# Kernel optimization log

Measured on AMD Instinct MI355X. Metric: run time of the kernel, lower is better.

The kernel has to match this reference:

```python
import jax, jax.numpy as jnp
import numpy as np

NUM_EDGE_TYPES = 8
HIDDEN = 128
N_NODES = 50000
N_EDGES = 600000


def setup_inputs() -> dict:
    key = jax.random.key(0)
    ks = jax.random.split(key, 10)
    H = HIDDEN
    h = jax.random.normal(ks[0], (N_NODES, H), dtype=jnp.float32)
    edge_index = jax.random.randint(ks[1], (2, N_EDGES), 0, N_NODES, dtype=jnp.int32)
    edge_type = jax.random.randint(ks[2], (N_EDGES,), 0, NUM_EDGE_TYPES + 1, dtype=jnp.int32)
    s = 1.0 / np.sqrt(H)
    W_msg = jax.random.uniform(ks[3], (H, H), jnp.float32, -s, s)
    b_msg = jax.random.uniform(ks[4], (H,), jnp.float32, -s, s)
    edge_embed = jax.random.normal(ks[5], (NUM_EDGE_TYPES + 1, H), dtype=jnp.float32)
    W_ih = jax.random.uniform(ks[6], (3 * H, H), jnp.float32, -s, s)
    W_hh = jax.random.uniform(ks[7], (3 * H, H), jnp.float32, -s, s)
    b_ih = jax.random.uniform(ks[8], (3 * H,), jnp.float32, -s, s)
    b_hh = jax.random.uniform(ks[9], (3 * H,), jnp.float32, -s, s)
    return {"h": h, "edge_index": edge_index, "edge_type": edge_type,
            "num_nodes": N_NODES, "W_msg": W_msg, "b_msg": b_msg,
            "edge_embed": edge_embed, "W_ih": W_ih, "W_hh": W_hh,
            "b_ih": b_ih, "b_hh": b_hh}


def _gru_cell(x, h, W_ih, W_hh, b_ih, b_hh):
    # PyTorch GRUCell: gates ordered (r, z, n)
    H = h.shape[-1]
    gi = x @ W_ih.T + b_ih  # (N, 3H)
    gh = h @ W_hh.T + b_hh
    i_r, i_z, i_n = gi[:, :H], gi[:, H:2 * H], gi[:, 2 * H:]
    h_r, h_z, h_n = gh[:, :H], gh[:, H:2 * H], gh[:, 2 * H:]
    r = jax.nn.sigmoid(i_r + h_r)
    z = jax.nn.sigmoid(i_z + h_z)
    n = jnp.tanh(i_n + r * h_n)
    return (1.0 - z) * n + z * h


def reference(h, edge_index, edge_type, num_nodes, W_msg, b_msg, edge_embed, W_ih, W_hh, b_ih, b_hh):
    src = edge_index[0]
    dst = edge_index[1]
    # gather -> linear -> edge-type embed add
    src_h = h[src] @ W_msg.T + b_msg                      # (E, H)
    emb = edge_embed[jnp.clip(edge_type, 0, NUM_EDGE_TYPES)]  # (E, H)
    msg = src_h + emb
    # scatter-add into per-node message buffer
    messages = jax.ops.segment_sum(msg, dst, num_segments=num_nodes)  # (num_nodes, H)
    h_new = _gru_cell(messages, h[:num_nodes], W_ih, W_hh, b_ih, b_hh)
    result = jnp.zeros_like(h).at[:num_nodes].set(h_new)
    return result
```

## Files before the change

kernel.cpp:

```cpp
#include <hip/hip_runtime.h>
#include <math.h>

#define H 128
typedef unsigned int u32;
typedef unsigned long long u64;
typedef __attribute__((ext_vector_type(8))) short short8;
typedef __attribute__((ext_vector_type(4))) float floatx4;

#define XS_STRIDE 136
#define CS_STRIDE 40

#define SCAN_B 64
#define SCAN_T 256

__device__ __forceinline__ float sigmoid_f(float x) {
    return 1.0f / (1.0f + __expf(-x));
}
__device__ __forceinline__ float tanh_f(float x) {
    float t = __expf(-2.0f * fabsf(x));
    float r = (1.0f - t) / (1.0f + t);
    return copysignf(r, x);
}
__device__ __forceinline__ unsigned short f2bf(float x) {
    u32 u = __float_as_uint(x);
    return (unsigned short)((u + 0x7fffu + ((u >> 16) & 1u)) >> 16);
}
__device__ __forceinline__ float bf2f(unsigned short s) {
    return __uint_as_float(((u32)s) << 16);
}
__device__ __forceinline__ float bf_lo32(u32 u) { return __uint_as_float(u << 16); }
__device__ __forceinline__ float bf_hi32(u32 u) { return __uint_as_float(u & 0xffff0000u); }

__global__ __launch_bounds__(256) void fused_pre_kernel(
    const float* __restrict__ h, unsigned short* __restrict__ h_b, int total8,
    int* __restrict__ deg, int N,
    const float* __restrict__ Wih, const float* __restrict__ Whh,
    const float* __restrict__ Wm,  const float* __restrict__ emb,
    const float* __restrict__ bm,
    unsigned short* __restrict__ Wcs, unsigned short* __restrict__ Whhs,
    unsigned short* __restrict__ embWs, int HB, int DB)
{
    int b = blockIdx.x;
    if (b < HB) {
        int idx = b * 256 + threadIdx.x;
        if (idx >= total8) return;
        const float4* p = (const float4*)(h + (size_t)idx * 8);
        float4 a = p[0], bb = p[1];
        short8 v;
        v[0] = (short)f2bf(a.x);  v[1] = (short)f2bf(a.y);
        v[2] = (short)f2bf(a.z);  v[3] = (short)f2bf(a.w);
        v[4] = (short)f2bf(bb.x); v[5] = (short)f2bf(bb.y);
        v[6] = (short)f2bf(bb.z); v[7] = (short)f2bf(bb.w);
        *(short8*)(h_b + (size_t)idx * 8) = v;
        return;
    }
    if (b < HB + DB) {
        int idx = (b - HB) * 256 + threadIdx.x;
        if (idx < N) deg[idx] = 0;
        return;
    }
    int idx = (b - HB - DB) * 256 + threadIdx.x;
    if (idx < 49152) {
        int g = idx >> 7;
        int k = idx & 127;
        float acc = 0.f;
#pragma unroll 4
        for (int c = 0; c < H; ++c)
            acc += Wih[(size_t)g * H + c] * Wm[(size_t)c * H + k];
        int gate = g >> 7;
        int wi = g & 127;
        int j = wi >> 4, m = wi & 15;
        int kc = k >> 5, q = (k >> 3) & 3, i = k & 7;
        int l = q * 16 + m;
        Wcs[(size_t)(((gate * 8 + j) * 4 + kc) * 64 + l) * 8 + i] = f2bf(acc);
    } else if (idx < 61440) {
        int s = idx - 49152;
        int i = s & 7;
        int l = (s >> 3) & 63;
        int jb = s >> 9;
        int gate = jb >> 3, jj = jb & 7;
        int q = l >> 4, m = l & 15;
        int t = q * 8 + i;
        unsigned short v = 0;
        if (t < 9) {
            int g = gate * 128 + jj * 16 + m;
            float acc = 0.f;
#pragma unroll 4
            for (int jx = 0; jx < H; ++jx)
                acc += (emb[(size_t)t * H + jx] + bm[jx]) * Wih[(size_t)g * H + jx];
            v = f2bf(acc);
        }
        embWs[s] = v;
    } else if (idx < 67584) {
        int t2 = idx - 61440;
        int l  = t2 & 63;
        int kc = (t2 >> 6) & 3;
        int jr = t2 >> 8;
        int m = l & 15, q = l >> 4;
        size_t srco = (size_t)(jr * 16 + m) * H + kc * 32 + q * 8;
        const float4* s0 = (const float4*)(Whh + srco);
        float4 a = s0[0], bb = s0[1];
        short8 v;
        v[0] = (short)f2bf(a.x);  v[1] = (short)f2bf(a.y);
        v[2] = (short)f2bf(a.z);  v[3] = (short)f2bf(a.w);
        v[4] = (short)f2bf(bb.x); v[5] = (short)f2bf(bb.y);
        v[6] = (short)f2bf(bb.z); v[7] = (short)f2bf(bb.w);
        *(short8*)(Whhs + (size_t)t2 * 8) = v;
    }
}

__global__ __launch_bounds__(256) void hist_kernel(
    const int* __restrict__ eidx, int* __restrict__ deg, int E)
{
    int e = blockIdx.x * 256 + threadIdx.x;
    if (e < E) atomicAdd(&deg[eidx[E + e]], 1);
}

__global__ __launch_bounds__(SCAN_T) void scan_part_kernel(
    const int* __restrict__ deg, int* __restrict__ tsum,
    int* __restrict__ bsum, int N, int ipt)
{
    __shared__ int red[SCAN_T];
    int t = threadIdx.x;
    int g = blockIdx.x * SCAN_T + t;
    int s = g * ipt;
    int e = s + ipt < N ? s + ipt : N;
    int sum = 0;
    for (int i = s; i < e; ++i) sum += deg[i];
    tsum[g] = sum;
    red[t] = sum;
    __syncthreads();
    for (int d = SCAN_T / 2; d > 0; d >>= 1) {
        if (t < d) red[t] += red[t + d];
        __syncthreads();
    }
    if (t == 0) bsum[blockIdx.x] = red[0];
}

__global__ __launch_bounds__(SCAN_T) void scan_final_kernel(
    const int* __restrict__ deg, const int* __restrict__ tsum,
    const int* __restrict__ bsum, int* __restrict__ off,
    int* __restrict__ pos, int N, int ipt)
{
    __shared__ int part[SCAN_T];
    __shared__ int bpre[SCAN_B + 1];
    int t = threadIdx.x;
    if (t == 0) {
        int acc = 0;
        for (int b2 = 0; b2 < SCAN_B; ++b2) { bpre[b2] = acc; acc += bsum[b2]; }
        bpre[SCAN_B] = acc;
        if (blockIdx.x == 0) off[N] = acc;
    }
    int g = blockIdx.x * SCAN_T + t;
    part[t] = tsum[g];
    __syncthreads();
    for (int d = 1; d < SCAN_T; d <<= 1) {
        int v = (t >= d) ? part[t - d] : 0;
        __syncthreads();
        part[t] += v;
        __syncthreads();
    }
    int base = bpre[blockIdx.x] + ((t == 0) ? 0 : part[t - 1]);
    int s = g * ipt;
    int e = s + ipt < N ? s + ipt : N;
    for (int i = s; i < e; ++i) {
        off[i] = base;
        pos[i] = base;
        base += deg[i];
    }
}

__global__ __launch_bounds__(256) void fill_kernel(
    const int* __restrict__ eidx, const int* __restrict__ etype,
    int* __restrict__ pos, int* __restrict__ packed, int E)
{
    int e = blockIdx.x * 256 + threadIdx.x;
    if (e >= E) return;
    int src = eidx[e];
    int dst = eidx[E + e];
    int t = etype[e];
    t = t < 0 ? 0 : (t > 8 ? 8 : t);
    int p = atomicAdd(&pos[dst], 1);
    packed[p] = src | (t << 24);
}

__global__ __launch_bounds__(256) void gather_kernel(
    const unsigned short* __restrict__ h_b,
    const int* __restrict__ off, const int* __restrict__ packed,
    unsigned short* __restrict__ S_b, u64* __restrict__ cnt, int N)
{
    int n = blockIdx.x * 4 + (threadIdx.x >> 6);
    if (n >= N) return;
    int lane = threadIdx.x & 63;
    int b = off[n], e = off[n + 1];
    float ax = 0.f, ay = 0.f;
    u64 c = 0;
    int i = b;
    for (; i + 8 <= e; i += 8) {
        int u0 = packed[i + 0];
        int u1 = packed[i + 1];
        int u2 = packed[i + 2];
        int u3 = packed[i + 3];
        int u4 = packed[i + 4];
        int u5 = packed[i + 5];
        int u6 = packed[i + 6];
        int u7 = packed[i + 7];
        u32 x0 = *((const u32*)(h_b + (size_t)(u0 & 0xffffff) * H) + lane);
        u32 x1 = *((const u32*)(h_b + (size_t)(u1 & 0xffffff) * H) + lane);
        u32 x2 = *((const u32*)(h_b + (size_t)(u2 & 0xffffff) * H) + lane);
        u32 x3 = *((const u32*)(h_b + (size_t)(u3 & 0xffffff) * H) + lane);
        u32 x4 = *((const u32*)(h_b + (size_t)(u4 & 0xffffff) * H) + lane);
        u32 x5 = *((const u32*)(h_b + (size_t)(u5 & 0xffffff) * H) + lane);
        u32 x6 = *((const u32*)(h_b + (size_t)(u6 & 0xffffff) * H) + lane);
        u32 x7 = *((const u32*)(h_b + (size_t)(u7 & 0xffffff) * H) + lane);
        c += (1ull << (7 * (u0 >> 24))) + (1ull << (7 * (u1 >> 24)))
           + (1ull << (7 * (u2 >> 24))) + (1ull << (7 * (u3 >> 24)))
           + (1ull << (7 * (u4 >> 24))) + (1ull << (7 * (u5 >> 24)))
           + (1ull << (7 * (u6 >> 24))) + (1ull << (7 * (u7 >> 24)));
        ax += bf_lo32(x0) + bf_lo32(x1) + bf_lo32(x2) + bf_lo32(x3)
            + bf_lo32(x4) + bf_lo32(x5) + bf_lo32(x6) + bf_lo32(x7);
        ay += bf_hi32(x0) + bf_hi32(x1) + bf_hi32(x2) + bf_hi32(x3)
            + bf_hi32(x4) + bf_hi32(x5) + bf_hi32(x6) + bf_hi32(x7);
    }
    for (; i + 4 <= e; i += 4) {
        int u0 = packed[i + 0];
        int u1 = packed[i + 1];
        int u2 = packed[i + 2];
        int u3 = packed[i + 3];
        u32 x0 = *((const u32*)(h_b + (size_t)(u0 & 0xffffff) * H) + lane);
        u32 x1 = *((const u32*)(h_b + (size_t)(u1 & 0xffffff) * H) + lane);
        u32 x2 = *((const u32*)(h_b + (size_t)(u2 & 0xffffff) * H) + lane);
        u32 x3 = *((const u32*)(h_b + (size_t)(u3 & 0xffffff) * H) + lane);
        c += (1ull << (7 * (u0 >> 24))) + (1ull << (7 * (u1 >> 24)))
           + (1ull << (7 * (u2 >> 24))) + (1ull << (7 * (u3 >> 24)));
        ax += bf_lo32(x0) + bf_lo32(x1) + bf_lo32(x2) + bf_lo32(x3);
        ay += bf_hi32(x0) + bf_hi32(x1) + bf_hi32(x2) + bf_hi32(x3);
    }
    for (; i < e; ++i) {
        int u = packed[i];
        u32 x = *((const u32*)(h_b + (size_t)(u & 0xffffff) * H) + lane);
        c += 1ull << (7 * (u >> 24));
        ax += bf_lo32(x);
        ay += bf_hi32(x);
    }
    u32 o = (u32)f2bf(ax) | ((u32)f2bf(ay) << 16);
    *((u32*)(S_b + (size_t)n * H) + lane) = o;
    if (lane == 0) cnt[n] = c;
}

__global__ __launch_bounds__(256, 4) void gru_mfma_kernel(
    const unsigned short* __restrict__ S_b, const unsigned short* __restrict__ h_b,
    const unsigned short* __restrict__ Wcs, const unsigned short* __restrict__ Whhs,
    const unsigned short* __restrict__ embWs,
    const float* __restrict__ bih, const float* __restrict__ bhh,
    const u64* __restrict__ cnt,
    const int* __restrict__ numn, float* __restrict__ out, int N)
{
    __shared__ unsigned short xs[64 * XS_STRIDE];
    __shared__ unsigned short hsb[64 * XS_STRIDE];
    __shared__ unsigned short cs[64 * CS_STRIDE];

    int tid = threadIdx.x;
    int bx = blockIdx.x;
    int node0 = (bx >> 1) * 64;
    int jhalf = bx & 1;

    int lane = tid & 63;
    int wv = tid >> 6;
    int j = jhalf * 4 + wv;

    short8 er = *(const short8*)(embWs + (size_t)((0 * 8 + j) * 64 + lane) * 8);
    short8 ez = *(const short8*)(embWs + (size_t)((1 * 8 + j) * 64 + lane) * 8);
    short8 en = *(const short8*)(embWs + (size_t)((2 * 8 + j) * 64 + lane) * 8);

    for (int c = tid; c < 1024; c += 256) {
        int r = c >> 4;
        int k8 = (c & 15) << 3;
        int n = node0 + r;
        int nc = n < N ? n : N - 1;
        *(short8*)(&xs[r * XS_STRIDE + k8]) =
            *(const short8*)(S_b + (size_t)nc * H + k8);
        *(short8*)(&hsb[r * XS_STRIDE + k8]) =
            *(const short8*)(h_b + (size_t)nc * H + k8);
    }
    {
        int r = tid >> 2, tg = tid & 3;
        int n = node0 + r;
        u64 cv = cnt[n < N ? n : N - 1];
        short8 v = {0, 0, 0, 0, 0, 0, 0, 0};
        if (tg == 0) {
#pragma unroll
            for (int i = 0; i < 8; ++i)
                v[i] = (short)f2bf((float)((u32)(cv >> (7 * i)) & 127u));
        } else if (tg == 1) {
            v[0] = (short)f2bf((float)((u32)(cv >> 56) & 127u));
        }
        *(short8*)(&cs[r * CS_STRIDE + tg * 8]) = v;
    }
    __syncthreads();

    int am = lane & 15;
    int aq = lane >> 4;

    int num_nodes = numn[0];
    floatx4 zero = {0.f, 0.f, 0.f, 0.f};

    floatx4 aR[4], aZ[4], aIn[4], aHn[4];
#pragma unroll
    for (int rt = 0; rt < 4; ++rt) {
        short8 acn = *(const short8*)(&cs[(rt * 16 + am) * CS_STRIDE + aq * 8]);
        aR[rt]  = __builtin_amdgcn_mfma_f32_16x16x32_bf16(acn, er, zero, 0, 0, 0);
        aZ[rt]  = __builtin_amdgcn_mfma_f32_16x16x32_bf16(acn, ez, zero, 0, 0, 0);
        aIn[rt] = __builtin_amdgcn_mfma_f32_16x16x32_bf16(acn, en, zero, 0, 0, 0);
        aHn[rt] = zero;
    }
#pragma unroll
    for (int kc = 0; kc < 4; ++kc) {
        size_t c_r = (size_t)(((0 * 8 + j) * 4 + kc) * 64 + lane) * 8;
        size_t c_z = (size_t)(((1 * 8 + j) * 4 + kc) * 64 + lane) * 8;
        size_t c_n = (size_t)(((2 * 8 + j) * 4 + kc) * 64 + lane) * 8;
        short8 bir = *(const short8*)(Wcs + c_r);
        short8 bhr = *(const short8*)(Whhs + c_r);
        short8 biz = *(const short8*)(Wcs + c_z);
        short8 bhz = *(const short8*)(Whhs + c_z);
        short8 bin = *(const short8*)(Wcs + c_n);
        short8 bhn = *(const short8*)(Whhs + c_n);
#pragma unroll
        for (int rt = 0; rt < 4; ++rt) {
            int arow = rt * 16 + am;
            short8 axv = *(const short8*)(&xs[arow * XS_STRIDE + kc * 32 + aq * 8]);
            short8 ahv = *(const short8*)(&hsb[arow * XS_STRIDE + kc * 32 + aq * 8]);
            aR[rt]  = __builtin_amdgcn_mfma_f32_16x16x32_bf16(axv, bir, aR[rt], 0, 0, 0);
            aR[rt]  = __builtin_amdgcn_mfma_f32_16x16x32_bf16(ahv, bhr, aR[rt], 0, 0, 0);
            aZ[rt]  = __builtin_amdgcn_mfma_f32_16x16x32_bf16(axv, biz, aZ[rt], 0, 0, 0);
            aZ[rt]  = __builtin_amdgcn_mfma_f32_16x16x32_bf16(ahv, bhz, aZ[rt], 0, 0, 0);
            aIn[rt] = __builtin_amdgcn_mfma_f32_16x16x32_bf16(axv, bin, aIn[rt], 0, 0, 0);
            aHn[rt] = __builtin_amdgcn_mfma_f32_16x16x32_bf16(ahv, bhn, aHn[rt], 0, 0, 0);
        }
    }
    int c = j * 16 + am;
    float b_r = bih[c]       + bhh[c];
    float b_z = bih[128 + c] + bhh[128 + c];
    float b_in = bih[256 + c], b_hn = bhh[256 + c];
#pragma unroll
    for (int rt = 0; rt < 4; ++rt) {
#pragma unroll
        for (int q = 0; q < 4; ++q) {
            int m = rt * 16 + aq * 4 + q;
            int node = node0 + m;
            if (node < N) {
                float r  = sigmoid_f(aR[rt][q] + b_r);
                float z  = sigmoid_f(aZ[rt][q] + b_z);
                float nv = tanh_f((aIn[rt][q] + b_in) + r * (aHn[rt][q] + b_hn));
                float hv = bf2f(hsb[m * XS_STRIDE + c]);
                float o  = (1.0f - z) * nv + z * hv;
                out[(size_t)node * H + c] = (node < num_nodes) ? o : 0.0f;
            }
        }
    }
}

extern "C" void kernel_launch(void* const* d_in, const int* in_sizes, int n_in,
                              void* d_out, int out_size, void* d_ws, size_t ws_size,
                              hipStream_t stream) {
    const float* h    = (const float*)d_in[0];
    const int*  eidx  = (const int*)d_in[1];
    const int*  etype = (const int*)d_in[2];
    const int*  numn  = (const int*)d_in[3];
    const float* Wm   = (const float*)d_in[4];
    const float* bm   = (const float*)d_in[5];
    const float* emb  = (const float*)d_in[6];
    const float* Wih  = (const float*)d_in[7];
    const float* Whh  = (const float*)d_in[8];
    const float* bih  = (const float*)d_in[9];
    const float* bhh  = (const float*)d_in[10];

    int N = in_sizes[0] / H;
    int E = in_sizes[2];

    unsigned short* S_b   = (unsigned short*)d_ws;
    unsigned short* h_b   = S_b + (size_t)N * H;
    unsigned short* Wcs   = h_b + (size_t)N * H;
    unsigned short* Whhs  = Wcs + 3 * H * H;
    unsigned short* embWs = Whhs + 3 * H * H;
    u64* cnt    = (u64*)(embWs + 12288);
    int* deg    = (int*)(cnt + N);
    int* pos    = deg + N;
    int* off    = pos + N;
    int* packed = off + (N + 1);
    int* tsum   = packed + E;
    int* bsum   = tsum + SCAN_B * SCAN_T;

    int total8 = N * H / 8;
    int HB = (total8 + 255) / 256;
    int DB = (N + 255) / 256;
    int PB = 264;
    fused_pre_kernel<<<HB + DB + PB, 256, 0, stream>>>(
        h, h_b, total8, deg, N, Wih, Whh, Wm, emb, bm, Wcs, Whhs, embWs, HB, DB);

    hist_kernel<<<(E + 255) / 256, 256, 0, stream>>>(eidx, deg, E);

    int ipt = (N + SCAN_B * SCAN_T - 1) / (SCAN_B * SCAN_T);
    scan_part_kernel<<<SCAN_B, SCAN_T, 0, stream>>>(deg, tsum, bsum, N, ipt);
    scan_final_kernel<<<SCAN_B, SCAN_T, 0, stream>>>(deg, tsum, bsum, off, pos, N, ipt);

    fill_kernel<<<(E + 255) / 256, 256, 0, stream>>>(eidx, etype, pos, packed, E);

    gather_kernel<<<(N + 3) / 4, 256, 0, stream>>>(h_b, off, packed, S_b, cnt, N);

    int nblk = ((N + 63) / 64) * 2;
    gru_mfma_kernel<<<nblk, 256, 0, stream>>>(S_b, h_b, Wcs, Whhs, embWs,
                                              bih, bhh, cnt, numn, (float*)d_out, N);
}
```

Measured before the change: 225.9 us.

## Fuse all stages into one cooperative persistent kernel with grid syncs

Replaces the seven separate launches (bf16 convert, histogram, two scan kernels, CSR fill, gather, GRU) with a single cooperative mega-kernel. It runs a grid-stride loop per stage, separated by grid.sync, and restructures the scan to use per-block sums. This removes per-launch overhead and inter-kernel gaps. The cost is a persistent grid of at most 512 blocks with launch bounds of 2 blocks per CU, which may lower occupancy for the memory-bound gather and GRU stages, plus several grid-wide barriers. The old multi-kernel path is kept as a fallback if the cooperative launch fails.

```diff
diff --git a/kernel.cpp b/kernel.cpp
--- a/kernel.cpp
+++ b/kernel.cpp
@@ -1,5 +1,8 @@
 #include <hip/hip_runtime.h>
+#include <hip/hip_cooperative_groups.h>
 #include <math.h>
+
+namespace cg = cooperative_groups;
 
 #define H 128
 typedef unsigned int u32;
@@ -31,35 +34,28 @@
 __device__ __forceinline__ float bf_lo32(u32 u) { return __uint_as_float(u << 16); }
 __device__ __forceinline__ float bf_hi32(u32 u) { return __uint_as_float(u & 0xffff0000u); }
 
-__global__ __launch_bounds__(256) void fused_pre_kernel(
-    const float* __restrict__ h, unsigned short* __restrict__ h_b, int total8,
-    int* __restrict__ deg, int N,
+
+__device__ __forceinline__ void conv8_item(
+    int idx, const float* __restrict__ h, unsigned short* __restrict__ h_b)
+{
+    const float4* p = (const float4*)(h + (size_t)idx * 8);
+    float4 a = p[0], bb = p[1];
+    short8 v;
+    v[0] = (short)f2bf(a.x);  v[1] = (short)f2bf(a.y);
+    v[2] = (short)f2bf(a.z);  v[3] = (short)f2bf(a.w);
+    v[4] = (short)f2bf(bb.x); v[5] = (short)f2bf(bb.y);
+    v[6] = (short)f2bf(bb.z); v[7] = (short)f2bf(bb.w);
+    *(short8*)(h_b + (size_t)idx * 8) = v;
+}
+
+__device__ __forceinline__ void prep_item(
+    int idx,
     const float* __restrict__ Wih, const float* __restrict__ Whh,
     const float* __restrict__ Wm,  const float* __restrict__ emb,
     const float* __restrict__ bm,
     unsigned short* __restrict__ Wcs, unsigned short* __restrict__ Whhs,
-    unsigned short* __restrict__ embWs, int HB, int DB)
-{
-    int b = blockIdx.x;
-    if (b < HB) {
-        int idx = b * 256 + threadIdx.x;
-        if (idx >= total8) return;
-        const float4* p = (const float4*)(h + (size_t)idx * 8);
-        float4 a = p[0], bb = p[1];
-        short8 v;
-        v[0] = (short)f2bf(a.x);  v[1] = (short)f2bf(a.y);
-        v[2] = (short)f2bf(a.z);  v[3] = (short)f2bf(a.w);
-        v[4] = (short)f2bf(bb.x); v[5] = (short)f2bf(bb.y);
-        v[6] = (short)f2bf(bb.z); v[7] = (short)f2bf(bb.w);
-        *(short8*)(h_b + (size_t)idx * 8) = v;
-        return;
-    }
-    if (b < HB + DB) {
-        int idx = (b - HB) * 256 + threadIdx.x;
-        if (idx < N) deg[idx] = 0;
-        return;
-    }
-    int idx = (b - HB - DB) * 256 + threadIdx.x;
+    unsigned short* __restrict__ embWs)
+{
     if (idx < 49152) {
         int g = idx >> 7;
         int k = idx & 127;
@@ -109,89 +105,12 @@
     }
 }
 
-__global__ __launch_bounds__(256) void hist_kernel(
-    const int* __restrict__ eidx, int* __restrict__ deg, int E)
-{
-    int e = blockIdx.x * 256 + threadIdx.x;
-    if (e < E) atomicAdd(&deg[eidx[E + e]], 1);
-}
-
-__global__ __launch_bounds__(SCAN_T) void scan_part_kernel(
-    const int* __restrict__ deg, int* __restrict__ tsum,
-    int* __restrict__ bsum, int N, int ipt)
-{
-    __shared__ int red[SCAN_T];
-    int t = threadIdx.x;
-    int g = blockIdx.x * SCAN_T + t;
-    int s = g * ipt;
-    int e = s + ipt < N ? s + ipt : N;
-    int sum = 0;
-    for (int i = s; i < e; ++i) sum += deg[i];
-    tsum[g] = sum;
-    red[t] = sum;
-    __syncthreads();
-    for (int d = SCAN_T / 2; d > 0; d >>= 1) {
-        if (t < d) red[t] += red[t + d];
-        __syncthreads();
-    }
-    if (t == 0) bsum[blockIdx.x] = red[0];
-}
-
-__global__ __launch_bounds__(SCAN_T) void scan_final_kernel(
-    const int* __restrict__ deg, const int* __restrict__ tsum,
-    const int* __restrict__ bsum, int* __restrict__ off,
-    int* __restrict__ pos, int N, int ipt)
-{
-    __shared__ int part[SCAN_T];
-    __shared__ int bpre[SCAN_B + 1];
-    int t = threadIdx.x;
-    if (t == 0) {
-        int acc = 0;
-        for (int b2 = 0; b2 < SCAN_B; ++b2) { bpre[b2] = acc; acc += bsum[b2]; }
-        bpre[SCAN_B] = acc;
-        if (blockIdx.x == 0) off[N] = acc;
-    }
-    int g = blockIdx.x * SCAN_T + t;
-    part[t] = tsum[g];
-    __syncthreads();
-    for (int d = 1; d < SCAN_T; d <<= 1) {
-        int v = (t >= d) ? part[t - d] : 0;
-        __syncthreads();
-        part[t] += v;
-        __syncthreads();
-    }
-    int base = bpre[blockIdx.x] + ((t == 0) ? 0 : part[t - 1]);
-    int s = g * ipt;
-    int e = s + ipt < N ? s + ipt : N;
-    for (int i = s; i < e; ++i) {
-        off[i] = base;
-        pos[i] = base;
-        base += deg[i];
-    }
-}
-
-__global__ __launch_bounds__(256) void fill_kernel(
-    const int* __restrict__ eidx, const int* __restrict__ etype,
-    int* __restrict__ pos, int* __restrict__ packed, int E)
-{
-    int e = blockIdx.x * 256 + threadIdx.x;
-    if (e >= E) return;
-    int src = eidx[e];
-    int dst = eidx[E + e];
-    int t = etype[e];
-    t = t < 0 ? 0 : (t > 8 ? 8 : t);
-    int p = atomicAdd(&pos[dst], 1);
-    packed[p] = src | (t << 24);
-}
-
-__global__ __launch_bounds__(256) void gather_kernel(
+__device__ __forceinline__ void gather_node(
+    int n, int lane,
     const unsigned short* __restrict__ h_b,
     const int* __restrict__ off, const int* __restrict__ packed,
-    unsigned short* __restrict__ S_b, u64* __restrict__ cnt, int N)
-{
-    int n = blockIdx.x * 4 + (threadIdx.x >> 6);
-    if (n >= N) return;
-    int lane = threadIdx.x & 63;
+    unsigned short* __restrict__ S_b, u64* __restrict__ cnt)
+{
     int b = off[n], e = off[n + 1];
     float ax = 0.f, ay = 0.f;
     u64 c = 0;
@@ -248,26 +167,21 @@
     if (lane == 0) cnt[n] = c;
 }
 
-__global__ __launch_bounds__(256, 4) void gru_mfma_kernel(
+__device__ __forceinline__ void gru_unit(
+    int node0, int jhalf, int tid,
+    unsigned short* xs, unsigned short* hsb, unsigned short* cs,
     const unsigned short* __restrict__ S_b, const unsigned short* __restrict__ h_b,
     const unsigned short* __restrict__ Wcs, const unsigned short* __restrict__ Whhs,
     const unsigned short* __restrict__ embWs,
     const float* __restrict__ bih, const float* __restrict__ bhh,
-    const u64* __restrict__ cnt,
-    const int* __restrict__ numn, float* __restrict__ out, int N)
-{
-    __shared__ unsigned short xs[64 * XS_STRIDE];
-    __shared__ unsigned short hsb[64 * XS_STRIDE];
-    __shared__ unsigned short cs[64 * CS_STRIDE];
-
-    int tid = threadIdx.x;
-    int bx = blockIdx.x;
-    int node0 = (bx >> 1) * 64;
-    int jhalf = bx & 1;
-
+    const u64* __restrict__ cnt, int num_nodes,
+    float* __restrict__ out, int N)
+{
     int lane = tid & 63;
     int wv = tid >> 6;
     int j = jhalf * 4 + wv;
+
+    __syncthreads();
 
     short8 er = *(const short8*)(embWs + (size_t)((0 * 8 + j) * 64 + lane) * 8);
     short8 ez = *(const short8*)(embWs + (size_t)((1 * 8 + j) * 64 + lane) * 8);
@@ -302,9 +216,7 @@
     int am = lane & 15;
     int aq = lane >> 4;
 
-    int num_nodes = numn[0];
     floatx4 zero = {0.f, 0.f, 0.f, 0.f};
-
     floatx4 aR[4], aZ[4], aIn[4], aHn[4];
 #pragma unroll
     for (int rt = 0; rt < 4; ++rt) {
@@ -360,6 +272,248 @@
     }
 }
 
+__global__ __launch_bounds__(256, 2) void mega_kernel(
+    const float* __restrict__ h, unsigned short* __restrict__ h_b, int total8,
+    const int* __restrict__ eidx, const int* __restrict__ etype, int E,
+    int* __restrict__ deg, int* __restrict__ off, int* __restrict__ pos,
+    int* __restrict__ packed, int* __restrict__ mbsum, int* __restrict__ mbpre,
+    const float* __restrict__ Wih, const float* __restrict__ Whh,
+    const float* __restrict__ Wm,  const float* __restrict__ emb,
+    const float* __restrict__ bm,
+    unsigned short* __restrict__ Wcs, unsigned short* __restrict__ Whhs,
+    unsigned short* __restrict__ embWs,
+    unsigned short* __restrict__ S_b, u64* __restrict__ cnt,
+    const float* __restrict__ bih, const float* __restrict__ bhh,
+    const int* __restrict__ numn, float* __restrict__ out, int N)
+{
+    __shared__ unsigned short xs[64 * XS_STRIDE];
+    __shared__ unsigned short hsb[64 * XS_STRIDE];
+    __shared__ unsigned short cs[64 * CS_STRIDE];
+
+    cg::grid_group grid = cg::this_grid();
+    int tid = threadIdx.x;
+    int nb  = gridDim.x;
+    int T   = nb * 256;
+    int gid = blockIdx.x * 256 + tid;
+
+    for (int idx = gid; idx < total8; idx += T) conv8_item(idx, h, h_b);
+    for (int idx = gid; idx < N; idx += T) deg[idx] = 0;
+    for (int idx = gid; idx < 67584; idx += T)
+        prep_item(idx, Wih, Whh, Wm, emb, bm, Wcs, Whhs, embWs);
+    __threadfence();
+    grid.sync();
+
+    for (int e = gid; e < E; e += T) atomicAdd(&deg[eidx[E + e]], 1);
+    __threadfence();
+    grid.sync();
+
+    int ipt = (N + T - 1) / T;
+    int* sscan = (int*)xs;
+    {
+        int s = gid * ipt;
+        int en = s + ipt < N ? s + ipt : N;
+        int sum = 0;
+        for (int i = s; i < en; ++i) sum += deg[i];
+        sscan[tid] = sum;
+        __syncthreads();
+        for (int d = 1; d < 256; d <<= 1) {
+            int v = (tid >= d) ? sscan[tid - d] : 0;
+            __syncthreads();
+            sscan[tid] += v;
+            __syncthreads();
+        }
+        if (tid == 255) mbsum[blockIdx.x] = sscan[255];
+    }
+    __threadfence();
+    grid.sync();
+
+    if (blockIdx.x == 0) {
+        int* ps = (int*)hsb;
+        int b0 = (2 * tid     < nb) ? mbsum[2 * tid]     : 0;
+        int b1 = (2 * tid + 1 < nb) ? mbsum[2 * tid + 1] : 0;
+        ps[tid] = b0 + b1;
+        __syncthreads();
+        for (int d = 1; d < 256; d <<= 1) {
+            int v = (tid >= d) ? ps[tid - d] : 0;
+            __syncthreads();
+            ps[tid] += v;
+            __syncthreads();
+        }
+        int excl_pair = tid ? ps[tid - 1] : 0;
+        if (2 * tid     < nb) mbpre[2 * tid]     = excl_pair;
+        if (2 * tid + 1 < nb) mbpre[2 * tid + 1] = excl_pair + b0;
+        if (tid == 255) off[N] = ps[255];
+    }
+    __threadfence();
+    grid.sync();
+
+    {
+        int base = mbpre[blockIdx.x] + (tid ? sscan[tid - 1] : 0);
+        int s = gid * ipt;
+        int en = s + ipt < N ? s + ipt : N;
+        for (int i = s; i < en; ++i) {
+            off[i] = base;
+            pos[i] = base;
+            base += deg[i];
+        }
+    }
+    __threadfence();
+    grid.sync();
+
+    for (int e = gid; e < E; e += T) {
+        int src = eidx[e];
+        int dst = eidx[E + e];
+        int t = etype[e];
+        t = t < 0 ? 0 : (t > 8 ? 8 : t);
+        int p = atomicAdd(&pos[dst], 1);
+        packed[p] = src | (t << 24);
+    }
+    __threadfence();
+    grid.sync();
+
+    {
+        int lane = tid & 63, wv = tid >> 6;
+        for (int n = blockIdx.x * 4 + wv; n < N; n += nb * 4)
+            gather_node(n, lane, h_b, off, packed, S_b, cnt);
+    }
+    __threadfence();
+    grid.sync();
+
+    {
+        int num_nodes = numn[0];
+        int nunits = ((N + 63) / 64) * 2;
+        for (int u = blockIdx.x; u < nunits; u += nb)
+            gru_unit((u >> 1) * 64, u & 1, tid, xs, hsb, cs,
+                     S_b, h_b, Wcs, Whhs, embWs, bih, bhh, cnt,
+                     num_nodes, out, N);
+    }
+}
+
+__global__ __launch_bounds__(256) void fused_pre_kernel(
+    const float* __restrict__ h, unsigned short* __restrict__ h_b, int total8,
+    int* __restrict__ deg, int N,
+    const float* __restrict__ Wih, const float* __restrict__ Whh,
+    const float* __restrict__ Wm,  const float* __restrict__ emb,
+    const float* __restrict__ bm,
+    unsigned short* __restrict__ Wcs, unsigned short* __restrict__ Whhs,
+    unsigned short* __restrict__ embWs, int HB, int DB)
+{
+    int b = blockIdx.x;
+    if (b < HB) {
+        int idx = b * 256 + threadIdx.x;
+        if (idx < total8) conv8_item(idx, h, h_b);
+        return;
+    }
+    if (b < HB + DB) {
+        int idx = (b - HB) * 256 + threadIdx.x;
+        if (idx < N) deg[idx] = 0;
+        return;
+    }
+    int idx = (b - HB - DB) * 256 + threadIdx.x;
+    prep_item(idx, Wih, Whh, Wm, emb, bm, Wcs, Whhs, embWs);
+}
+
+__global__ __launch_bounds__(256) void hist_kernel(
+    const int* __restrict__ eidx, int* __restrict__ deg, int E)
+{
+    int e = blockIdx.x * 256 + threadIdx.x;
+    if (e < E) atomicAdd(&deg[eidx[E + e]], 1);
+}
+
+__global__ __launch_bounds__(SCAN_T) void scan_part_kernel(
+    const int* __restrict__ deg, int* __restrict__ tsum,
+    int* __restrict__ bsum, int N, int ipt)
+{
+    __shared__ int red[SCAN_T];
+    int t = threadIdx.x;
+    int g = blockIdx.x * SCAN_T + t;
+    int s = g * ipt;
+    int e = s + ipt < N ? s + ipt : N;
+    int sum = 0;
+    for (int i = s; i < e; ++i) sum += deg[i];
+    tsum[g] = sum;
+    red[t] = sum;
+    __syncthreads();
+    for (int d = SCAN_T / 2; d > 0; d >>= 1) {
+        if (t < d) red[t] += red[t + d];
+        __syncthreads();
+    }
+    if (t == 0) bsum[blockIdx.x] = red[0];
+}
+
+__global__ __launch_bounds__(SCAN_T) void scan_final_kernel(
+    const int* __restrict__ deg, const int* __restrict__ tsum,
+    const int* __restrict__ bsum, int* __restrict__ off,
+    int* __restrict__ pos, int N, int ipt)
+{
+    __shared__ int part[SCAN_T];
+    __shared__ int bpre[SCAN_B + 1];
+    int t = threadIdx.x;
+    if (t == 0) {
+        int acc = 0;
+        for (int b2 = 0; b2 < SCAN_B; ++b2) { bpre[b2] = acc; acc += bsum[b2]; }
+        bpre[SCAN_B] = acc;
+        if (blockIdx.x == 0) off[N] = acc;
+    }
+    int g = blockIdx.x * SCAN_T + t;
+    part[t] = tsum[g];
+    __syncthreads();
+    for (int d = 1; d < SCAN_T; d <<= 1) {
+        int v = (t >= d) ? part[t - d] : 0;
+        __syncthreads();
+        part[t] += v;
+        __syncthreads();
+    }
+    int base = bpre[blockIdx.x] + ((t == 0) ? 0 : part[t - 1]);
+    int s = g * ipt;
+    int e = s + ipt < N ? s + ipt : N;
+    for (int i = s; i < e; ++i) {
+        off[i] = base;
+        pos[i] = base;
+        base += deg[i];
+    }
+}
+
+__global__ __launch_bounds__(256) void fill_kernel(
+    const int* __restrict__ eidx, const int* __restrict__ etype,
+    int* __restrict__ pos, int* __restrict__ packed, int E)
+{
+    int e = blockIdx.x * 256 + threadIdx.x;
+    if (e >= E) return;
+    int src = eidx[e];
+    int dst = eidx[E + e];
+    int t = etype[e];
+    t = t < 0 ? 0 : (t > 8 ? 8 : t);
+    int p = atomicAdd(&pos[dst], 1);
+    packed[p] = src | (t << 24);
+}
+
+__global__ __launch_bounds__(256) void gather_kernel(
+    const unsigned short* __restrict__ h_b,
+    const int* __restrict__ off, const int* __restrict__ packed,
+    unsigned short* __restrict__ S_b, u64* __restrict__ cnt, int N)
+{
+    int n = blockIdx.x * 4 + (threadIdx.x >> 6);
+    if (n >= N) return;
+    gather_node(n, threadIdx.x & 63, h_b, off, packed, S_b, cnt);
+}
+
+__global__ __launch_bounds__(256, 4) void gru_mfma_kernel(
+    const unsigned short* __restrict__ S_b, const unsigned short* __restrict__ h_b,
+    const unsigned short* __restrict__ Wcs, const unsigned short* __restrict__ Whhs,
+    const unsigned short* __restrict__ embWs,
+    const float* __restrict__ bih, const float* __restrict__ bhh,
+    const u64* __restrict__ cnt,
+    const int* __restrict__ numn, float* __restrict__ out, int N)
+{
+    __shared__ unsigned short xs[64 * XS_STRIDE];
+    __shared__ unsigned short hsb[64 * XS_STRIDE];
+    __shared__ unsigned short cs[64 * CS_STRIDE];
+    int bx = blockIdx.x;
+    gru_unit((bx >> 1) * 64, bx & 1, threadIdx.x, xs, hsb, cs,
+             S_b, h_b, Wcs, Whhs, embWs, bih, bhh, cnt, numn[0], out, N);
+}
+
 extern "C" void kernel_launch(void* const* d_in, const int* in_sizes, int n_in,
                               void* d_out, int out_size, void* d_ws, size_t ws_size,
                               hipStream_t stream) {
@@ -390,25 +544,71 @@
     int* packed = off + (N + 1);
     int* tsum   = packed + E;
     int* bsum   = tsum + SCAN_B * SCAN_T;
+    int* mbsum  = tsum;
+    int* mbpre  = tsum + 1024;
+    float* outp = (float*)d_out;
 
     int total8 = N * H / 8;
-    int HB = (total8 + 255) / 256;
-    int DB = (N + 255) / 256;
-    int PB = 264;
-    fused_pre_kernel<<<HB + DB + PB, 256, 0, stream>>>(
-        h, h_b, total8, deg, N, Wih, Whh, Wm, emb, bm, Wcs, Whhs, embWs, HB, DB);
-
-    hist_kernel<<<(E + 255) / 256, 256, 0, stream>>>(eidx, deg, E);
-
-    int ipt = (N + SCAN_B * SCAN_T - 1) / (SCAN_B * SCAN_T);
-    scan_part_kernel<<<SCAN_B, SCAN_T, 0, stream>>>(deg, tsum, bsum, N, ipt);
-    scan_final_kernel<<<SCAN_B, SCAN_T, 0, stream>>>(deg, tsum, bsum, off, pos, N, ipt);
-
-    fill_kernel<<<(E + 255) / 256, 256, 0, stream>>>(eidx, etype, pos, packed, E);
-
-    gather_kernel<<<(N + 3) / 4, 256, 0, stream>>>(h_b, off, packed, S_b, cnt, N);
-
-    int nblk = ((N + 63) / 64) * 2;
-    gru_mfma_kernel<<<nblk, 256, 0, stream>>>(S_b, h_b, Wcs, Whhs, embWs,
-                                              bih, bhh, cnt, numn, (float*)d_out, N);
-}
+
+    static int coop_grid = -2;
+    if (coop_grid == -2) {
+        int nbpc = 0;
+        hipError_t e1 = hipOccupancyMaxActiveBlocksPerMultiprocessor(
+            &nbpc, mega_kernel, 256, 0);
+        int ncu = 0;
+        hipDeviceProp_t prop;
+        if (hipGetDeviceProperties(&prop, 0) == hipSuccess)
+            ncu = prop.multiProcessorCount;
+        if (e1 == hipSuccess && nbpc > 0 && ncu > 0) {
+            long g = (long)nbpc * (long)ncu;
+            coop_grid = (int)(g > 512 ? 512 : g);
+        } else {
+            coop_grid = -1;
+        }
+    }
+
+    bool done = false;
+    if (coop_grid > 0) {
+        void* kargs[] = {
+            (void*)&h, (void*)&h_b, (void*)&total8,
+            (void*)&eidx, (void*)&etype, (void*)&E,
+            (void*)&deg, (void*)&off, (void*)&pos, (void*)&packed,
+            (void*)&mbsum, (void*)&mbpre,
+            (void*)&Wih, (void*)&Whh, (void*)&Wm, (void*)&emb, (void*)&bm,
+            (void*)&Wcs, (void*)&Whhs, (void*)&embWs,
+            (void*)&S_b, (void*)&cnt,
+            (void*)&bih, (void*)&bhh, (void*)&numn,
+            (void*)&outp, (void*)&N
+        };
+        hipError_t err = hipLaunchCooperativeKernel(
+            (void*)mega_kernel, dim3((unsigned)coop_grid), dim3(256),
+            kargs, 0u, stream);
+        if (err == hipSuccess) {
+            done = true;
+        } else {
+            coop_grid = -1;
+        }
+    }
+
+    if (!done) {
+        int HB = (total8 + 255) / 256;
+        int DB = (N + 255) / 256;
+        int PB = 264;
+        fused_pre_kernel<<<HB + DB + PB, 256, 0, stream>>>(
+            h, h_b, total8, deg, N, Wih, Whh, Wm, emb, bm, Wcs, Whhs, embWs, HB, DB);
+
+        hist_kernel<<<(E + 255) / 256, 256, 0, stream>>>(eidx, deg, E);
+
+        int ipt = (N + SCAN_B * SCAN_T - 1) / (SCAN_B * SCAN_T);
+        scan_part_kernel<<<SCAN_B, SCAN_T, 0, stream>>>(deg, tsum, bsum, N, ipt);
+        scan_final_kernel<<<SCAN_B, SCAN_T, 0, stream>>>(deg, tsum, bsum, off, pos, N, ipt);
+
+        fill_kernel<<<(E + 255) / 256, 256, 0, stream>>>(eidx, etype, pos, packed, E);
+
+        gather_kernel<<<(N + 3) / 4, 256, 0, stream>>>(h_b, off, packed, S_b, cnt, N);
+
+        int nblk = ((N + 63) / 64) * 2;
+        gru_mfma_kernel<<<nblk, 256, 0, stream>>>(S_b, h_b, Wcs, Whhs, embWs,
+                                                  bih, bhh, cnt, numn, outp, N);
+    }
+}
```

Result: slower. 679.3 us (+200.8%).

## Replace CSR build with fixed-capacity per-node buckets plus overflow linked list

Applied to the files above, without the earlier changes.

Drops the histogram, two-pass scan and separate fill kernels. Edges are now written straight into a per-destination slot array of capacity 64, indexed by an atomic counter, and edges beyond that capacity go onto an atomic linked list. The gather kernel reads each node's slot row and walks the overflow list only when needed. This removes three kernel launches and their serialized scan passes. In exchange it uses a larger N*64 slot buffer with sparser row reads, makes accumulation order nondeterministic, and serializes the overflow walk for high-degree nodes.

```diff
diff --git a/kernel.cpp b/kernel.cpp
--- a/kernel.cpp
+++ b/kernel.cpp
@@ -9,9 +9,7 @@
 
 #define XS_STRIDE 136
 #define CS_STRIDE 40
-
-#define SCAN_B 64
-#define SCAN_T 256
+#define CAP 64
 
 __device__ __forceinline__ float sigmoid_f(float x) {
     return 1.0f / (1.0f + __expf(-x));
@@ -33,7 +31,7 @@
 
 __global__ __launch_bounds__(256) void fused_pre_kernel(
     const float* __restrict__ h, unsigned short* __restrict__ h_b, int total8,
-    int* __restrict__ deg, int N,
+    int* __restrict__ deg, int* __restrict__ ohead, int N,
     const float* __restrict__ Wih, const float* __restrict__ Whh,
     const float* __restrict__ Wm,  const float* __restrict__ emb,
     const float* __restrict__ bm,
@@ -57,6 +55,7 @@
     if (b < HB + DB) {
         int idx = (b - HB) * 256 + threadIdx.x;
         if (idx < N) deg[idx] = 0;
+        else if (idx < 2 * N) ohead[idx - N] = -1;
         return;
     }
     int idx = (b - HB - DB) * 256 + threadIdx.x;
@@ -109,70 +108,11 @@
     }
 }
 
-__global__ __launch_bounds__(256) void hist_kernel(
-    const int* __restrict__ eidx, int* __restrict__ deg, int E)
-{
-    int e = blockIdx.x * 256 + threadIdx.x;
-    if (e < E) atomicAdd(&deg[eidx[E + e]], 1);
-}
-
-__global__ __launch_bounds__(SCAN_T) void scan_part_kernel(
-    const int* __restrict__ deg, int* __restrict__ tsum,
-    int* __restrict__ bsum, int N, int ipt)
-{
-    __shared__ int red[SCAN_T];
-    int t = threadIdx.x;
-    int g = blockIdx.x * SCAN_T + t;
-    int s = g * ipt;
-    int e = s + ipt < N ? s + ipt : N;
-    int sum = 0;
-    for (int i = s; i < e; ++i) sum += deg[i];
-    tsum[g] = sum;
-    red[t] = sum;
-    __syncthreads();
-    for (int d = SCAN_T / 2; d > 0; d >>= 1) {
-        if (t < d) red[t] += red[t + d];
-        __syncthreads();
-    }
-    if (t == 0) bsum[blockIdx.x] = red[0];
-}
-
-__global__ __launch_bounds__(SCAN_T) void scan_final_kernel(
-    const int* __restrict__ deg, const int* __restrict__ tsum,
-    const int* __restrict__ bsum, int* __restrict__ off,
-    int* __restrict__ pos, int N, int ipt)
-{
-    __shared__ int part[SCAN_T];
-    __shared__ int bpre[SCAN_B + 1];
-    int t = threadIdx.x;
-    if (t == 0) {
-        int acc = 0;
-        for (int b2 = 0; b2 < SCAN_B; ++b2) { bpre[b2] = acc; acc += bsum[b2]; }
-        bpre[SCAN_B] = acc;
-        if (blockIdx.x == 0) off[N] = acc;
-    }
-    int g = blockIdx.x * SCAN_T + t;
-    part[t] = tsum[g];
-    __syncthreads();
-    for (int d = 1; d < SCAN_T; d <<= 1) {
-        int v = (t >= d) ? part[t - d] : 0;
-        __syncthreads();
-        part[t] += v;
-        __syncthreads();
-    }
-    int base = bpre[blockIdx.x] + ((t == 0) ? 0 : part[t - 1]);
-    int s = g * ipt;
-    int e = s + ipt < N ? s + ipt : N;
-    for (int i = s; i < e; ++i) {
-        off[i] = base;
-        pos[i] = base;
-        base += deg[i];
-    }
-}
-
-__global__ __launch_bounds__(256) void fill_kernel(
+__global__ __launch_bounds__(256) void fill_bucket_kernel(
     const int* __restrict__ eidx, const int* __restrict__ etype,
-    int* __restrict__ pos, int* __restrict__ packed, int E)
+    int* __restrict__ deg, int* __restrict__ slots,
+    int* __restrict__ ohead, int* __restrict__ onext,
+    int* __restrict__ packed, int E)
 {
     int e = blockIdx.x * 256 + threadIdx.x;
     if (e >= E) return;
@@ -180,31 +120,43 @@
     int dst = eidx[E + e];
     int t = etype[e];
     t = t < 0 ? 0 : (t > 8 ? 8 : t);
-    int p = atomicAdd(&pos[dst], 1);
-    packed[p] = src | (t << 24);
-}
-
-__global__ __launch_bounds__(256) void gather_kernel(
+    int enc = src | (t << 24);
+    int p = atomicAdd(&deg[dst], 1);
+    if (p < CAP) {
+        slots[(size_t)dst * CAP + p] = enc;
+    } else {
+        packed[e] = enc;
+        int old = atomicExch(&ohead[dst], e);
+        onext[e] = old;
+    }
+}
+
+__global__ __launch_bounds__(256) void gather_bucket_kernel(
     const unsigned short* __restrict__ h_b,
-    const int* __restrict__ off, const int* __restrict__ packed,
+    const int* __restrict__ deg, const int* __restrict__ slots,
+    const int* __restrict__ ohead, const int* __restrict__ onext,
+    const int* __restrict__ packed,
     unsigned short* __restrict__ S_b, u64* __restrict__ cnt, int N)
 {
     int n = blockIdx.x * 4 + (threadIdx.x >> 6);
     if (n >= N) return;
     int lane = threadIdx.x & 63;
-    int b = off[n], e = off[n + 1];
+    int dcnt = deg[n];
+    int m = dcnt < CAP ? dcnt : CAP;
+    const int* row = slots + (size_t)n * CAP;
+
     float ax = 0.f, ay = 0.f;
     u64 c = 0;
-    int i = b;
-    for (; i + 8 <= e; i += 8) {
-        int u0 = packed[i + 0];
-        int u1 = packed[i + 1];
-        int u2 = packed[i + 2];
-        int u3 = packed[i + 3];
-        int u4 = packed[i + 4];
-        int u5 = packed[i + 5];
-        int u6 = packed[i + 6];
-        int u7 = packed[i + 7];
+    int i = 0;
+    for (; i + 8 <= m; i += 8) {
+        int u0 = row[i + 0];
+        int u1 = row[i + 1];
+        int u2 = row[i + 2];
+        int u3 = row[i + 3];
+        int u4 = row[i + 4];
+        int u5 = row[i + 5];
+        int u6 = row[i + 6];
+        int u7 = row[i + 7];
         u32 x0 = *((const u32*)(h_b + (size_t)(u0 & 0xffffff) * H) + lane);
         u32 x1 = *((const u32*)(h_b + (size_t)(u1 & 0xffffff) * H) + lane);
         u32 x2 = *((const u32*)(h_b + (size_t)(u2 & 0xffffff) * H) + lane);
@@ -222,11 +174,11 @@
         ay += bf_hi32(x0) + bf_hi32(x1) + bf_hi32(x2) + bf_hi32(x3)
             + bf_hi32(x4) + bf_hi32(x5) + bf_hi32(x6) + bf_hi32(x7);
     }
-    for (; i + 4 <= e; i += 4) {
-        int u0 = packed[i + 0];
-        int u1 = packed[i + 1];
-        int u2 = packed[i + 2];
-        int u3 = packed[i + 3];
+    for (; i + 4 <= m; i += 4) {
+        int u0 = row[i + 0];
+        int u1 = row[i + 1];
+        int u2 = row[i + 2];
+        int u3 = row[i + 3];
         u32 x0 = *((const u32*)(h_b + (size_t)(u0 & 0xffffff) * H) + lane);
         u32 x1 = *((const u32*)(h_b + (size_t)(u1 & 0xffffff) * H) + lane);
         u32 x2 = *((const u32*)(h_b + (size_t)(u2 & 0xffffff) * H) + lane);
@@ -236,12 +188,23 @@
         ax += bf_lo32(x0) + bf_lo32(x1) + bf_lo32(x2) + bf_lo32(x3);
         ay += bf_hi32(x0) + bf_hi32(x1) + bf_hi32(x2) + bf_hi32(x3);
     }
-    for (; i < e; ++i) {
-        int u = packed[i];
+    for (; i < m; ++i) {
+        int u = row[i];
         u32 x = *((const u32*)(h_b + (size_t)(u & 0xffffff) * H) + lane);
         c += 1ull << (7 * (u >> 24));
         ax += bf_lo32(x);
         ay += bf_hi32(x);
+    }
+    if (dcnt > CAP) {
+        int ecur = ohead[n];
+        while (ecur >= 0) {
+            int u = packed[ecur];
+            u32 x = *((const u32*)(h_b + (size_t)(u & 0xffffff) * H) + lane);
+            c += 1ull << (7 * (u >> 24));
+            ax += bf_lo32(x);
+            ay += bf_hi32(x);
+            ecur = onext[ecur];
+        }
     }
     u32 o = (u32)f2bf(ax) | ((u32)f2bf(ay) << 16);
     *((u32*)(S_b + (size_t)n * H) + lane) = o;
@@ -385,28 +348,24 @@
     unsigned short* embWs = Whhs + 3 * H * H;
     u64* cnt    = (u64*)(embWs + 12288);
     int* deg    = (int*)(cnt + N);
-    int* pos    = deg + N;
-    int* off    = pos + N;
-    int* packed = off + (N + 1);
-    int* tsum   = packed + E;
-    int* bsum   = tsum + SCAN_B * SCAN_T;
+    int* ohead  = deg + N;
+    int* slots  = ohead + N;
+    int* packed = slots + (size_t)N * CAP;
+    int* onext  = packed + E;
 
     int total8 = N * H / 8;
     int HB = (total8 + 255) / 256;
-    int DB = (N + 255) / 256;
+    int DB = (2 * N + 255) / 256;
     int PB = 264;
     fused_pre_kernel<<<HB + DB + PB, 256, 0, stream>>>(
-        h, h_b, total8, deg, N, Wih, Whh, Wm, emb, bm, Wcs, Whhs, embWs, HB, DB);
-
-    hist_kernel<<<(E + 255) / 256, 256, 0, stream>>>(eidx, deg, E);
-
-    int ipt = (N + SCAN_B * SCAN_T - 1) / (SCAN_B * SCAN_T);
-    scan_part_kernel<<<SCAN_B, SCAN_T, 0, stream>>>(deg, tsum, bsum, N, ipt);
-    scan_final_kernel<<<SCAN_B, SCAN_T, 0, stream>>>(deg, tsum, bsum, off, pos, N, ipt);
-
-    fill_kernel<<<(E + 255) / 256, 256, 0, stream>>>(eidx, etype, pos, packed, E);
-
-    gather_kernel<<<(N + 3) / 4, 256, 0, stream>>>(h_b, off, packed, S_b, cnt, N);
+        h, h_b, total8, deg, ohead, N, Wih, Whh, Wm, emb, bm, Wcs, Whhs, embWs,
+        HB, DB);
+
+    fill_bucket_kernel<<<(E + 255) / 256, 256, 0, stream>>>(
+        eidx, etype, deg, slots, ohead, onext, packed, E);
+
+    gather_bucket_kernel<<<(N + 3) / 4, 256, 0, stream>>>(
+        h_b, deg, slots, ohead, onext, packed, S_b, cnt, N);
 
     int nblk = ((N + 63) / 64) * 2;
     gru_mfma_kernel<<<nblk, 256, 0, stream>>>(S_b, h_b, Wcs, Whhs, embWs,
```

Result: faster. 194.7 us (-13.8%).
